# Kernel tuning notes

Measured on AMD Instinct MI355X. Metric: run time of the kernel, lower is better.

The kernel has to match this reference:

```python
import jax, jax.numpy as jnp
import numpy as np

N, D, E = 100000, 128, 1600000
BN_EPS = 1e-5

def setup_inputs() -> dict:
    key = jax.random.key(0)
    k1, k2, k3 = jax.random.split(key, 3)
    src_embeddings = jax.random.normal(k1, (N, D), dtype=jnp.float32)
    dst_embeddings = jax.random.normal(k2, (N, D), dtype=jnp.float32)
    graph = jax.random.randint(k3, (2, E), 0, N, dtype=jnp.int64)
    bn_weight = jnp.ones((1,), dtype=jnp.float32)
    bn_bias = jnp.zeros((1,), dtype=jnp.float32)
    return {
        "src_embeddings": src_embeddings,
        "dst_embeddings": dst_embeddings,
        "graph": graph,
        "bn_weight": bn_weight,
        "bn_bias": bn_bias,
    }

def reference(src_embeddings, dst_embeddings, graph, bn_weight, bn_bias):
    # gather endpoint embeddings by edge indices: [E, D]
    src = src_embeddings[graph[0]]
    dst = dst_embeddings[graph[1]]
    # squared distance per edge, clamped as in torch .clamp(min=1e-12)
    d2 = jnp.clip(jnp.sum((src - dst) ** 2, axis=-1), 1e-12, None)  # [E]
    likelihood = -jnp.log(d2)
    # BatchNorm1d(1) in training mode: batch mean, biased variance, eps=1e-5
    mu = jnp.mean(likelihood)
    var = jnp.mean((likelihood - mu) ** 2)
    edge_weights_logits = bn_weight[0] * (likelihood - mu) * jax.lax.rsqrt(var + BN_EPS) + bn_bias[0]
    # weighting_function = torch.sigmoid
    edge_weights = jax.nn.sigmoid(edge_weights_logits)
    # normalize=True: divide by mean
    edge_weights = edge_weights / jnp.mean(edge_weights)
    edge_weights = edge_weights[:, None]  # [E, 1]
    return graph, edge_weights, edge_weights_logits
```

## Files before the change

### kernel.cpp

```cpp
#include <hip/hip_runtime.h>
#include <math.h>

#define EMB_D 128
#define BN_EPS 1e-5f
#define CHUNK 6144
#define RUN_TILE 128

#define QSCALE 22.0f
#define INV_QS2 (1.0f / (QSCALE * QSCALE))

typedef float v4f __attribute__((ext_vector_type(4)));

#if defined(__has_builtin)
#if __has_builtin(__builtin_amdgcn_sdot4)
#define SDOT4_HW 1
#endif
#endif

__device__ __forceinline__ int sdot4i(unsigned int a, unsigned int b, int c) {
#ifdef SDOT4_HW
    return __builtin_amdgcn_sdot4((int)a, (int)b, c, false);
#else
    int s = c;
    s += (((int)a << 24) >> 24) * (((int)b << 24) >> 24);
    s += (((int)a << 16) >> 24) * (((int)b << 16) >> 24);
    s += (((int)a << 8)  >> 24) * (((int)b << 8)  >> 24);
    s += ((int)a >> 24) * ((int)b >> 24);
    return s;
#endif
}

__device__ __forceinline__ unsigned int q4(float4 v) {
    const int a = (int)rintf(fminf(fmaxf(v.x * QSCALE, -127.0f), 127.0f));
    const int b = (int)rintf(fminf(fmaxf(v.y * QSCALE, -127.0f), 127.0f));
    const int c = (int)rintf(fminf(fmaxf(v.z * QSCALE, -127.0f), 127.0f));
    const int d = (int)rintf(fminf(fmaxf(v.w * QSCALE, -127.0f), 127.0f));
    return (unsigned int)(a & 0xff) | ((unsigned int)(b & 0xff) << 8)
         | ((unsigned int)(c & 0xff) << 16) | ((unsigned int)(d & 0xff) << 24);
}

__device__ __forceinline__ int d2_dword(unsigned int a, unsigned int b, int m) {
    const int pab = sdot4i(a, b, 0);
    m = sdot4i(a, a, m);
    m = sdot4i(b, b, m);
    return m - 2 * pab;
}

__global__ void prep_bin_kernel(const float* __restrict__ src,
                                const float* __restrict__ dst,
                                unsigned int* __restrict__ src8,
                                unsigned int* __restrict__ dst8,
                                long long N,
                                const int* __restrict__ g,
                                long long E,
                                float* __restrict__ out_graph,
                                unsigned int* __restrict__ rec32,
                                unsigned short* __restrict__ boff,
                                unsigned short* __restrict__ inv16,
                                long long nchunks,
                                int slice_sz,
                                float inv_slice,
                                double* __restrict__ acc)
{
    if (blockIdx.x == 0 && threadIdx.x == 0) {
        acc[0] = 0.0; acc[1] = 0.0; acc[2] = 0.0; acc[3] = 0.0;
    }

    const long long nthreads = (long long)gridDim.x * blockDim.x;
    const long long tid0 = (long long)blockIdx.x * blockDim.x + threadIdx.x;

    {
        const long long nvec = N * 32;
        for (long long i = tid0; i < nvec; i += nthreads)
            src8[i] = q4(((const float4*)src)[i]);
        for (long long i = tid0; i < nvec; i += nthreads)
            dst8[i] = q4(((const float4*)dst)[i]);
    }

    __shared__ unsigned int hist[64];
    __shared__ unsigned int curs[64];

    for (long long c = blockIdx.x; c < nchunks; c += gridDim.x) {
        const long long base = c * CHUNK;
        const int cnt = (int)((E - base) < CHUNK ? (E - base) : CHUNK);

        if (threadIdx.x < 64) hist[threadIdx.x] = 0;
        __syncthreads();

        for (int t = threadIdx.x; t < cnt; t += blockDim.x) {
            const long long e = base + t;
            const unsigned int s = (unsigned int)g[e];
            const unsigned int d = (unsigned int)g[E + e];
            int bs = (int)((float)s * inv_slice); bs = bs > 7 ? 7 : bs;
            int bd = (int)((float)d * inv_slice); bd = bd > 7 ? 7 : bd;
            atomicAdd(&hist[bs * 8 + bd], 1u);
        }
        __syncthreads();

        if (threadIdx.x < 64) {
            const unsigned int v = hist[threadIdx.x];
            unsigned int inc = v;
            #pragma unroll
            for (int ofs = 1; ofs < 64; ofs <<= 1) {
                const unsigned int o = __shfl_up(inc, ofs, 64);
                if ((int)threadIdx.x >= ofs) inc += o;
            }
            const unsigned int excl = inc - v;
            curs[threadIdx.x] = excl;
            boff[c * 64 + threadIdx.x] = (unsigned short)excl;
        }
        __syncthreads();

        for (int t = threadIdx.x; t < cnt; t += blockDim.x) {
            const long long e = base + t;
            const unsigned int s = (unsigned int)g[e];
            const unsigned int d = (unsigned int)g[E + e];
            __builtin_nontemporal_store((float)s, &out_graph[e]);
            __builtin_nontemporal_store((float)d, &out_graph[E + e]);
            int bs = (int)((float)s * inv_slice); bs = bs > 7 ? 7 : bs;
            int bd = (int)((float)d * inv_slice); bd = bd > 7 ? 7 : bd;
            const int b = bs * 8 + bd;
            const unsigned int pos = atomicAdd(&curs[b], 1u);
            const unsigned int sl = s - (unsigned int)(bs * slice_sz);
            const unsigned int dl = d - (unsigned int)(bd * slice_sz);
            rec32[base + pos] = sl | (dl << 14);
            inv16[e] = (unsigned short)pos;
        }
        __syncthreads();
    }
}

__global__ void edge_l_binned_kernel(const uint4* __restrict__ src8,
                                     const uint4* __restrict__ dst8,
                                     const unsigned int* __restrict__ rec32,
                                     const unsigned short* __restrict__ boff,
                                     long long nchunks,
                                     long long E,
                                     int slice_sz,
                                     float* __restrict__ L_rec,
                                     double* __restrict__ acc)
{
    const int tid = threadIdx.x;
    const int sub = tid & 7;
    const int grp = tid >> 3;
    const int xcd = (int)(blockIdx.x & 7);
    const unsigned int bloc = blockIdx.x >> 3;
    const unsigned int B = gridDim.x >> 3;
    const int sBase = xcd * slice_sz;

    double sumL = 0.0, sumL2 = 0.0;

    for (int j = 0; j < 8; ++j) {
        const int b = xcd * 8 + j;
        const int dBase = j * slice_sz;

        for (long long c = bloc; c < nchunks; c += B) {
            const long long base = c * CHUNK;
            const int cnt = (int)((E - base) < CHUNK ? (E - base) : CHUNK);
            const int start = (int)boff[c * 64 + b];
            const int end = (b == 63) ? cnt : (int)boff[c * 64 + b + 1];
            const int len = end - start;
            const long long rbase = base + start;

            for (int t0 = 0; t0 < len; t0 += RUN_TILE) {
                bool ok[4];
                int tt[4], ss[4], dd[4];
                #pragma unroll
                for (int q = 0; q < 4; ++q) {
                    const int t = t0 + grp + q * 32;
                    ok[q] = t < len;
                    tt[q] = ok[q] ? t : 0;
                    const unsigned int r = rec32[rbase + tt[q]];
                    ss[q] = sBase + (int)(r & 0x3FFFu);
                    dd[q] = dBase + (int)((r >> 14) & 0x3FFFu);
                }

                int mq[4];
                #pragma unroll
                for (int q = 0; q < 4; ++q) {
                    const uint4 A = src8[(long long)ss[q] * 8 + sub];
                    const uint4 Bv = dst8[(long long)dd[q] * 8 + sub];
                    int m = d2_dword(A.x, Bv.x, 0);
                    m = d2_dword(A.y, Bv.y, m);
                    m = d2_dword(A.z, Bv.z, m);
                    m = d2_dword(A.w, Bv.w, m);
                    mq[q] = m;
                }
                #pragma unroll
                for (int q = 0; q < 4; ++q) {
                    mq[q] += __shfl_xor(mq[q], 1, 64);
                    mq[q] += __shfl_xor(mq[q], 2, 64);
                    mq[q] += __shfl_xor(mq[q], 4, 64);
                }

                if (sub == 0) {
                    #pragma unroll
                    for (int q = 0; q < 4; ++q) {
                        if (ok[q]) {
                            const float d2 = (float)mq[q] * INV_QS2;
                            const float L = -logf(fmaxf(d2, 1e-12f));
                            L_rec[rbase + tt[q]] = L;
                            sumL  += (double)L;
                            sumL2 += (double)L * (double)L;
                        }
                    }
                }
            }
        }
    }

    __shared__ double sA[256];
    __shared__ double sB[256];
    sA[tid] = sumL;
    sB[tid] = sumL2;
    __syncthreads();
    for (int ofs = 128; ofs >= 1; ofs >>= 1) {
        if (tid < ofs) {
            sA[tid] += sA[tid + ofs];
            sB[tid] += sB[tid + ofs];
        }
        __syncthreads();
    }
    if (tid == 0) {
        atomicAdd(&acc[0], sA[0]);
        atomicAdd(&acc[1], sB[0]);
    }
}

__global__ void sig_sum_kernel(const float* __restrict__ L_rec,
                               long long E,
                               const double* __restrict__ acc,
                               double* __restrict__ sig_acc,
                               const float* __restrict__ bn_w,
                               const float* __restrict__ bn_b)
{
    const long long nthreads = (long long)gridDim.x * blockDim.x;
    const long long tid0 = (long long)blockIdx.x * blockDim.x + threadIdx.x;

    __shared__ float s_mu, s_inv, s_w, s_b;
    if (threadIdx.x == 0) {
        const double mu  = acc[0] / (double)E;
        const double var = acc[1] / (double)E - mu * mu;
        s_mu  = (float)mu;
        s_inv = (float)(1.0 / sqrt(var + (double)BN_EPS));
        s_w   = bn_w[0];
        s_b   = bn_b[0];
    }
    __syncthreads();
    const float mu = s_mu, iv = s_inv, w = s_w, b = s_b;

    double sig = 0.0;
    const long long nvec = E / 4;
    for (long long i = tid0; i < nvec; i += nthreads) {
        const float4 L = ((const float4*)L_rec)[i];
        const float z0 = w * (L.x - mu) * iv + b;
        const float z1 = w * (L.y - mu) * iv + b;
        const float z2 = w * (L.z - mu) * iv + b;
        const float z3 = w * (L.w - mu) * iv + b;
        const float sx = 1.0f / (1.0f + expf(-z0));
        const float sy = 1.0f / (1.0f + expf(-z1));
        const float sz = 1.0f / (1.0f + expf(-z2));
        const float sw2 = 1.0f / (1.0f + expf(-z3));
        sig += (double)(sx + sy) + (double)(sz + sw2);
    }
    for (long long i = nvec * 4 + tid0; i < E; i += nthreads) {
        const float z = w * (L_rec[i] - mu) * iv + b;
        sig += (double)(1.0f / (1.0f + expf(-z)));
    }

    __shared__ double sS[256];
    sS[threadIdx.x] = sig;
    __syncthreads();
    for (int ofs = 128; ofs >= 1; ofs >>= 1) {
        if ((int)threadIdx.x < ofs)
            sS[threadIdx.x] += sS[threadIdx.x + ofs];
        __syncthreads();
    }
    if (threadIdx.x == 0)
        atomicAdd(sig_acc, sS[0]);
}

__global__ void finalize_kernel(const unsigned short* __restrict__ inv16,
                                const float* __restrict__ L_rec,
                                float* __restrict__ logits,
                                float* __restrict__ ew,
                                const double* __restrict__ acc,
                                const double* __restrict__ sig_acc,
                                const float* __restrict__ bn_w,
                                const float* __restrict__ bn_b,
                                long long E,
                                long long nchunks)
{
    __shared__ float Ls[CHUNK];
    __shared__ float s_mu, s_inv, s_w, s_b, s_scale;
    if (threadIdx.x == 0) {
        const double mu  = acc[0] / (double)E;
        const double var = acc[1] / (double)E - mu * mu;
        s_mu  = (float)mu;
        s_inv = (float)(1.0 / sqrt(var + (double)BN_EPS));
        s_w   = bn_w[0];
        s_b   = bn_b[0];
        s_scale = (float)((double)E / sig_acc[0]);
    }
    __syncthreads();
    const float mu = s_mu, iv = s_inv, w = s_w, b = s_b, scale = s_scale;

    for (long long c = blockIdx.x; c < nchunks; c += gridDim.x) {
        const long long base = c * CHUNK;
        const int cnt = (int)((E - base) < CHUNK ? (E - base) : CHUNK);

        __syncthreads();
        for (int t = threadIdx.x; t < cnt; t += blockDim.x)
            Ls[t] = L_rec[base + t];
        __syncthreads();

        for (int t = threadIdx.x; t < cnt; t += blockDim.x) {
            const long long e = base + t;
            const float z = w * (Ls[inv16[e]] - mu) * iv + b;
            __builtin_nontemporal_store(z, &logits[e]);
            __builtin_nontemporal_store(scale / (1.0f + expf(-z)), &ew[e]);
        }
    }
}

__global__ void prep_kernel(const float* __restrict__ src,
                            const float* __restrict__ dst,
                            unsigned int* __restrict__ src8,
                            unsigned int* __restrict__ dst8,
                            long long N,
                            const int* __restrict__ g,
                            long long E,
                            float* __restrict__ out_graph)
{
    const long long nthreads = (long long)gridDim.x * blockDim.x;
    const long long tid0 = (long long)blockIdx.x * blockDim.x + threadIdx.x;
    const long long nvec = N * 32;

    for (long long i = tid0; i < nvec; i += nthreads)
        src8[i] = q4(((const float4*)src)[i]);
    for (long long i = tid0; i < nvec; i += nthreads)
        dst8[i] = q4(((const float4*)dst)[i]);

    const long long gvec = (2 * E) / 4;
    for (long long i = tid0; i < gvec; i += nthreads) {
        const int4 v = ((const int4*)g)[i];
        v4f f;
        f.x = (float)v.x; f.y = (float)v.y; f.z = (float)v.z; f.w = (float)v.w;
        __builtin_nontemporal_store(f, (v4f*)out_graph + i);
    }
    for (long long i = gvec * 4 + tid0; i < 2 * E; i += nthreads)
        out_graph[i] = (float)g[i];
}

__global__ void edge_l_i8_kernel(const uint4* __restrict__ src8,
                                 const uint4* __restrict__ dst8,
                                 const int* __restrict__ g,
                                 long long E,
                                 float* __restrict__ l_out,
                                 double* __restrict__ acc)
{
    const int tid = threadIdx.x;
    const int sub = tid & 7;
    const int grp = tid >> 3;
    const long long blkSpan = 64;
    const long long stride = (long long)gridDim.x * blkSpan;

    double sumL = 0.0, sumL2 = 0.0;

    for (long long base = (long long)blockIdx.x * blkSpan; base < E; base += stride) {
        const long long e1 = base + (long long)grp * 2;
        const long long e2 = e1 + 1;
        const bool ok1 = e1 < E;
        const bool ok2 = e2 < E;

        int s1 = 0, d1 = 0, s2 = 0, d2i = 0;
        if (ok1) { s1 = g[e1]; d1 = g[E + e1]; }
        if (ok2) { s2 = g[e2]; d2i = g[E + e2]; }

        const uint4 A1 = src8[(long long)s1 * 8 + sub];
        const uint4 B1 = dst8[(long long)d1 * 8 + sub];
        const uint4 A2 = src8[(long long)s2 * 8 + sub];
        const uint4 B2 = dst8[(long long)d2i * 8 + sub];

        int m1 = d2_dword(A1.x, B1.x, 0);
        m1 = d2_dword(A1.y, B1.y, m1);
        m1 = d2_dword(A1.z, B1.z, m1);
        m1 = d2_dword(A1.w, B1.w, m1);
        int m2 = d2_dword(A2.x, B2.x, 0);
        m2 = d2_dword(A2.y, B2.y, m2);
        m2 = d2_dword(A2.z, B2.z, m2);
        m2 = d2_dword(A2.w, B2.w, m2);

        m1 += __shfl_xor(m1, 1, 64);
        m1 += __shfl_xor(m1, 2, 64);
        m1 += __shfl_xor(m1, 4, 64);
        m2 += __shfl_xor(m2, 1, 64);
        m2 += __shfl_xor(m2, 2, 64);
        m2 += __shfl_xor(m2, 4, 64);

        if (sub == 0) {
            if (ok1) {
                const float L = -logf(fmaxf((float)m1 * INV_QS2, 1e-12f));
                l_out[e1] = L;
                sumL  += (double)L;
                sumL2 += (double)L * (double)L;
            }
            if (ok2) {
                const float L = -logf(fmaxf((float)m2 * INV_QS2, 1e-12f));
                l_out[e2] = L;
                sumL  += (double)L;
                sumL2 += (double)L * (double)L;
            }
        }
    }

    __shared__ double sA[256];
    __shared__ double sB[256];
    sA[tid] = sumL;
    sB[tid] = sumL2;
    __syncthreads();
    for (int ofs = 128; ofs >= 1; ofs >>= 1) {
        if (tid < ofs) {
            sA[tid] += sA[tid + ofs];
            sB[tid] += sB[tid + ofs];
        }
        __syncthreads();
    }
    if (tid == 0) {
        atomicAdd(&acc[0], sA[0]);
        atomicAdd(&acc[1], sB[0]);
    }
}

__global__ void edge_l_kernel(const float* __restrict__ src,
                              const float* __restrict__ dst,
                              const int*   __restrict__ g,
                              long long E,
                              float*  __restrict__ l_out,
                              double* __restrict__ acc)
{
    const int sub  = threadIdx.x & 7;
    const int egrp = threadIdx.x >> 3;
    const long long stride = (long long)gridDim.x * 32;

    double sumL = 0.0, sumL2 = 0.0;

    long long e = (long long)blockIdx.x * 32 + egrp;
    int s = 0, d = 0;
    if (e < E) { s = g[e]; d = g[E + e]; }

    while (e < E) {
        const long long en = e + stride;
        int sn = 0, dn = 0;
        if (en < E) { sn = g[en]; dn = g[E + en]; }

        const float4* sa = (const float4*)(src + (long long)s * EMB_D);
        const float4* sb = (const float4*)(dst + (long long)d * EMB_D);
        const float4 a0 = sa[sub];      const float4 b0 = sb[sub];
        const float4 a1 = sa[sub + 8];  const float4 b1 = sb[sub + 8];
        const float4 a2 = sa[sub + 16]; const float4 b2 = sb[sub + 16];
        const float4 a3 = sa[sub + 24]; const float4 b3 = sb[sub + 24];

        float dx, dy, dz, dw, p = 0.f;
        dx = a0.x-b0.x; dy = a0.y-b0.y; dz = a0.z-b0.z; dw = a0.w-b0.w;
        p += fmaf(dx,dx,fmaf(dy,dy,fmaf(dz,dz,dw*dw)));
        dx = a1.x-b1.x; dy = a1.y-b1.y; dz = a1.z-b1.z; dw = a1.w-b1.w;
        p += fmaf(dx,dx,fmaf(dy,dy,fmaf(dz,dz,dw*dw)));
        dx = a2.x-b2.x; dy = a2.y-b2.y; dz = a2.z-b2.z; dw = a2.w-b2.w;
        p += fmaf(dx,dx,fmaf(dy,dy,fmaf(dz,dz,dw*dw)));
        dx = a3.x-b3.x; dy = a3.y-b3.y; dz = a3.z-b3.z; dw = a3.w-b3.w;
        p += fmaf(dx,dx,fmaf(dy,dy,fmaf(dz,dz,dw*dw)));

        p += __shfl_xor(p, 1, 64);
        p += __shfl_xor(p, 2, 64);
        p += __shfl_xor(p, 4, 64);

        if (sub == 0) {
            const float L = -logf(fmaxf(p, 1e-12f));
            l_out[e] = L;
            sumL  += (double)L;
            sumL2 += (double)L * (double)L;
        }
        e = en; s = sn; d = dn;
    }

    __shared__ double sA[256];
    __shared__ double sB[256];
    sA[threadIdx.x] = sumL;
    sB[threadIdx.x] = sumL2;
    __syncthreads();
    for (int ofs = 128; ofs >= 1; ofs >>= 1) {
        if ((int)threadIdx.x < ofs) {
            sA[threadIdx.x] += sA[threadIdx.x + ofs];
            sB[threadIdx.x] += sB[threadIdx.x + ofs];
        }
        __syncthreads();
    }
    if (threadIdx.x == 0) {
        atomicAdd(&acc[0], sA[0]);
        atomicAdd(&acc[1], sB[0]);
    }
}

__global__ void graph_copy_kernel(const int* __restrict__ g,
                                  float* __restrict__ out_graph,
                                  long long E2)
{
    const long long nth = (long long)gridDim.x * blockDim.x;
    for (long long i = (long long)blockIdx.x * blockDim.x + threadIdx.x;
         i < E2; i += nth)
        out_graph[i] = (float)g[i];
}

__global__ void bn_sig_kernel(float* __restrict__ logits,
                              const double* __restrict__ acc,
                              double* __restrict__ sig_acc,
                              const float* __restrict__ bn_w,
                              const float* __restrict__ bn_b,
                              long long E)
{
    const long long nthreads = (long long)gridDim.x * blockDim.x;
    const long long tid0 = (long long)blockIdx.x * blockDim.x + threadIdx.x;

    __shared__ float s_mu, s_inv, s_w, s_b;
    if (threadIdx.x == 0) {
        const double mu  = acc[0] / (double)E;
        const double var = acc[1] / (double)E - mu * mu;
        s_mu  = (float)mu;
        s_inv = (float)(1.0 / sqrt(var + (double)BN_EPS));
        s_w   = bn_w[0];
        s_b   = bn_b[0];
    }
    __syncthreads();
    const float mu = s_mu, inv = s_inv, w = s_w, b = s_b;

    double sig = 0.0;
    const long long nvec = E / 4;
    for (long long i = tid0; i < nvec; i += nthreads) {
        float4 L = ((const float4*)logits)[i];
        float4 z;
        z.x = w * (L.x - mu) * inv + b;
        z.y = w * (L.y - mu) * inv + b;
        z.z = w * (L.z - mu) * inv + b;
        z.w = w * (L.w - mu) * inv + b;
        ((float4*)logits)[i] = z;
        const float sx = 1.0f / (1.0f + expf(-z.x));
        const float sy = 1.0f / (1.0f + expf(-z.y));
        const float sz = 1.0f / (1.0f + expf(-z.z));
        const float sw2 = 1.0f / (1.0f + expf(-z.w));
        sig += (double)(sx + sy) + (double)(sz + sw2);
    }
    for (long long i = nvec * 4 + tid0; i < E; i += nthreads) {
        const float L = logits[i];
        const float z = w * (L - mu) * inv + b;
        logits[i] = z;
        sig += (double)(1.0f / (1.0f + expf(-z)));
    }

    __shared__ double sS[256];
    sS[threadIdx.x] = sig;
    __syncthreads();
    for (int ofs = 128; ofs >= 1; ofs >>= 1) {
        if ((int)threadIdx.x < ofs)
            sS[threadIdx.x] += sS[threadIdx.x + ofs];
        __syncthreads();
    }
    if (threadIdx.x == 0)
        atomicAdd(sig_acc, sS[0]);
}

__global__ void norm_kernel(const float* __restrict__ logits,
                            float* __restrict__ ew,
                            const double* __restrict__ sig_acc,
                            long long E)
{
    const long long nthreads = (long long)gridDim.x * blockDim.x;
    const long long tid0 = (long long)blockIdx.x * blockDim.x + threadIdx.x;
    const float scale = (float)((double)E / sig_acc[0]);

    const long long nvec = E / 4;
    for (long long i = tid0; i < nvec; i += nthreads) {
        const float4 z = ((const float4*)logits)[i];
        v4f v;
        v.x = scale / (1.0f + expf(-z.x));
        v.y = scale / (1.0f + expf(-z.y));
        v.z = scale / (1.0f + expf(-z.z));
        v.w = scale / (1.0f + expf(-z.w));
        __builtin_nontemporal_store(v, (v4f*)ew + i);
    }
    for (long long i = nvec * 4 + tid0; i < E; i += nthreads)
        ew[i] = scale / (1.0f + expf(-logits[i]));
}

extern "C" void kernel_launch(void* const* d_in, const int* in_sizes, int n_in,
                              void* d_out, int out_size, void* d_ws, size_t ws_size,
                              hipStream_t stream) {
    const float* src  = (const float*)d_in[0];
    const float* dst  = (const float*)d_in[1];
    const int*   g    = (const int*)d_in[2];
    const float* bn_w = (const float*)d_in[3];
    const float* bn_b = (const float*)d_in[4];

    const long long N = (long long)in_sizes[0] / EMB_D;
    const long long E = (long long)in_sizes[2] / 2;

    float* out        = (float*)d_out;
    float* out_graph  = out;
    float* out_ew     = out + 2 * E;
    float* out_logits = out + 3 * E;

    const long long nchunks = (E + CHUNK - 1) / CHUNK;
    const long long SLOTS = nchunks * CHUNK;

    double*       acc  = (double*)d_ws;
    unsigned char* src8 = (unsigned char*)d_ws + 512;
    unsigned char* dst8 = src8 + (size_t)N * EMB_D;
    unsigned int* rec32 = (unsigned int*)(dst8 + (size_t)N * EMB_D);
    float* L_rec = (float*)(rec32 + SLOTS);
    unsigned short* inv16 = (unsigned short*)(L_rec + SLOTS);
    unsigned short* boff  = inv16 + SLOTS;

    const size_t need_t3 = 512 + (size_t)N * EMB_D * 2;
    const size_t need_t1 = need_t3 + (size_t)SLOTS * 10 + (size_t)nchunks * 128;

    const int slice_sz = (int)((N + 7) / 8);
    const float inv_slice = 1.0f / (float)slice_sz;
    const bool pack_ok = (slice_sz < 16384) && (E < (1LL << 31));

    if (ws_size >= need_t1 && pack_ok) {
        prep_bin_kernel<<<4096, 256, 0, stream>>>(src, dst,
                                                  (unsigned int*)src8,
                                                  (unsigned int*)dst8,
                                                  N, g, E, out_graph,
                                                  rec32, boff, inv16,
                                                  nchunks, slice_sz, inv_slice,
                                                  acc);
        edge_l_binned_kernel<<<2048, 256, 0, stream>>>(
            (const uint4*)src8, (const uint4*)dst8, rec32, boff,
            nchunks, E, slice_sz, L_rec, acc);
        sig_sum_kernel<<<1024, 256, 0, stream>>>(L_rec, E, acc, &acc[2],
                                                 bn_w, bn_b);
        finalize_kernel<<<(unsigned int)nchunks, 256, 0, stream>>>(
            inv16, L_rec, out_logits, out_ew, acc, &acc[2],
            bn_w, bn_b, E, nchunks);
    } else if (ws_size >= need_t3) {
        (void)hipMemsetAsync(d_ws, 0, 512, stream);
        prep_kernel<<<4096, 256, 0, stream>>>(src, dst,
                                              (unsigned int*)src8,
                                              (unsigned int*)dst8,
                                              N, g, E, out_graph);
        edge_l_i8_kernel<<<4096, 256, 0, stream>>>((const uint4*)src8,
                                                   (const uint4*)dst8,
                                                   g, E, out_logits, acc);
        bn_sig_kernel<<<1024, 256, 0, stream>>>(out_logits, acc, &acc[2],
                                                bn_w, bn_b, E);
        norm_kernel<<<1024, 256, 0, stream>>>(out_logits, out_ew, &acc[2], E);
    } else {
        (void)hipMemsetAsync(d_ws, 0, 512, stream);
        edge_l_kernel<<<4096, 256, 0, stream>>>(src, dst, g, E, out_logits, acc);
        bn_sig_kernel<<<1024, 256, 0, stream>>>(out_logits, acc, &acc[2],
                                                bn_w, bn_b, E);
        norm_kernel<<<1024, 256, 0, stream>>>(out_logits, out_ew, &acc[2], E);
        graph_copy_kernel<<<1024, 256, 0, stream>>>(g, out_graph, 2 * E);
    }
}
```

Before: 270.9 us.

## Prefetch embedding slices into cache cooperatively before each binned edge pass

Before processing each destination bin, each block streams its share of the source slice and the current destination slice with coalesced loads, so the XCD-local L2 is warmed before the random gathers run. L_rec is written with nontemporal stores so the output does not evict the embeddings, and the finalize kernel launch doubles its block size. The warm-up adds extra memory traffic, and if finalize_kernel assumes 256 threads per block, the larger launch could misbehave.

```diff
diff --git a/kernel.cpp b/kernel.cpp
--- a/kernel.cpp
+++ b/kernel.cpp
@@ -136,6 +136,7 @@
                                      const unsigned short* __restrict__ boff,
                                      long long nchunks,
                                      long long E,
+                                     long long N,
                                      int slice_sz,
                                      float* __restrict__ L_rec,
                                      double* __restrict__ acc)
@@ -147,12 +148,40 @@
     const unsigned int bloc = blockIdx.x >> 3;
     const unsigned int B = gridDim.x >> 3;
     const int sBase = xcd * slice_sz;
+    const long long NV = N * 8;
 
     double sumL = 0.0, sumL2 = 0.0;
+    unsigned int sink = 0;
+
+    {
+        const long long v0 = (long long)sBase * 8;
+        long long v1 = v0 + (long long)slice_sz * 8;
+        if (v1 > NV) v1 = NV;
+        const long long seg = (v1 - v0 + B - 1) / B;
+        const long long p0 = v0 + (long long)bloc * seg;
+        long long p1 = p0 + seg; if (p1 > v1) p1 = v1;
+        for (long long p = p0 + tid; p < p1; p += blockDim.x) {
+            const uint4 v = src8[p];
+            sink ^= v.x ^ v.y ^ v.z ^ v.w;
+        }
+    }
 
     for (int j = 0; j < 8; ++j) {
         const int b = xcd * 8 + j;
         const int dBase = j * slice_sz;
+
+        {
+            const long long v0 = (long long)dBase * 8;
+            long long v1 = v0 + (long long)slice_sz * 8;
+            if (v1 > NV) v1 = NV;
+            const long long seg = (v1 - v0 + B - 1) / B;
+            const long long p0 = v0 + (long long)bloc * seg;
+            long long p1 = p0 + seg; if (p1 > v1) p1 = v1;
+            for (long long p = p0 + tid; p < p1; p += blockDim.x) {
+                const uint4 v = dst8[p];
+                sink ^= v.x ^ v.y ^ v.z ^ v.w;
+            }
+        }
 
         for (long long c = bloc; c < nchunks; c += B) {
             const long long base = c * CHUNK;
@@ -199,7 +228,7 @@
                         if (ok[q]) {
                             const float d2 = (float)mq[q] * INV_QS2;
                             const float L = -logf(fmaxf(d2, 1e-12f));
-                            L_rec[rbase + tt[q]] = L;
+                            __builtin_nontemporal_store(L, &L_rec[rbase + tt[q]]);
                             sumL  += (double)L;
                             sumL2 += (double)L * (double)L;
                         }
@@ -208,6 +237,8 @@
             }
         }
     }
+
+    asm volatile("" :: "v"(sink));
 
     __shared__ double sA[256];
     __shared__ double sB[256];
@@ -637,10 +668,10 @@
                                                   acc);
         edge_l_binned_kernel<<<2048, 256, 0, stream>>>(
             (const uint4*)src8, (const uint4*)dst8, rec32, boff,
-            nchunks, E, slice_sz, L_rec, acc);
+            nchunks, E, N, slice_sz, L_rec, acc);
         sig_sum_kernel<<<1024, 256, 0, stream>>>(L_rec, E, acc, &acc[2],
                                                  bn_w, bn_b);
-        finalize_kernel<<<(unsigned int)nchunks, 256, 0, stream>>>(
+        finalize_kernel<<<(unsigned int)nchunks, 512, 0, stream>>>(
             inv16, L_rec, out_logits, out_ew, acc, &acc[2],
             bn_w, bn_b, E, nchunks);
     } else if (ws_size >= need_t3) {
```

New measurement: 273.4 us. About the same (+0.9%).
